# Optimization experiments

Measured on AMD Instinct MI355X. Metric: run time of the kernel, lower is better.

The kernel has to match this reference:

```python
import jax, jax.numpy as jnp
import numpy as np

INTERVAL = 4
UPSCALE = 4
K = 3              # sample_size
SAMPLERS = 3
Q = 2 ** INTERVAL                 # 16
L = 2 ** (8 - INTERVAL) + 1       # 17
PAD = K - 1
B, H, W = 4, 512, 512

_STRIDES = np.array([L ** 3, L ** 2, L, 1], dtype=np.int32)


def ste_round(x):
    # straight-through round (round_func in the torch code)
    return x + jax.lax.stop_gradient(jnp.round(x) - x)


def fix_weight(w):
    return jnp.clip(ste_round(w * 127.0), -127.0, 127.0)


def sample(img, sw, sb):
    # unfold(K, K-1) + conv-per-patch + fold is exactly a VALID conv.
    # img: (B,1,h+PAD,w+PAD); sw: (4,1,K,K) -> a,b,c,d each (B,1,h,w)
    out = jax.lax.conv_general_dilated(img, sw, (1, 1), 'VALID',
        dimension_numbers=('NCHW', 'OIHW', 'NCHW')) + sb[None, :, None, None]
    return out[:, 0:1], out[:, 1:2], out[:, 2:3], out[:, 3:4]


def interp(lut, res_w, sw, sb, scale, img_in, prev_img):
    # InterpTorchBatch: 4D simplex interpolation into the quantized LUT.
    # Sorted-simplex form is equivalent to the 24-case masked torch code
    # (ties yield zero-weight terms, so tie ordering is irrelevant).
    w = fix_weight(lut)                                       # (L^4, scale*scale)
    a, b, c, d = sample(img_in, sw, sb)
    if prev_img is not None:
        rw = jnp.clip(res_w, 0.0, 1.0)
        pa, pb, pc, pd = sample(prev_img, sw, sb)
        a = rw[0, 0] * pa + (1.0 - rw[0, 0]) * a
        b = rw[0, 1] * pb + (1.0 - rw[0, 1]) * b
        c = rw[1, 0] * pc + (1.0 - rw[1, 0]) * c
        d = rw[1, 1] * pd + (1.0 - rw[1, 1]) * d
    vals = jnp.concatenate([a, b, c, d], axis=1).transpose(0, 2, 3, 1)   # (B,h,w,4)
    lo = jnp.floor_divide(vals, float(Q)).astype(jnp.int32)
    f = jnp.mod(vals, float(Q))
    order = jnp.argsort(-f, axis=-1)                          # fractional parts, descending
    fs = jnp.take_along_axis(f, order, axis=-1)
    strides = jnp.asarray(_STRIDES)
    base = jnp.sum(lo * strides, axis=-1)                     # flat index of p0000
    inc = jnp.cumsum(strides[order], axis=-1)
    verts = jnp.concatenate([base[..., None], base[..., None] + inc], axis=-1)  # (B,h,w,5)
    ws = jnp.concatenate([float(Q) - fs[..., :1], fs[..., :-1] - fs[..., 1:], fs[..., -1:]], axis=-1)
    p = w[verts]                                              # gather: (B,h,w,5,scale*scale)
    out = jnp.einsum('bhwv,bhwvk->bhwk', ws, p) / float(Q)
    bb, hh, ww, _ = out.shape
    out = out.reshape(bb, hh, ww, scale, scale).transpose(0, 1, 3, 2, 4)
    return out.reshape(bb, 1, hh * scale, ww * scale)


def _pad_rot(x, r):
    return jnp.pad(jnp.rot90(x, r, axes=(2, 3)),
                   ((0, 0), (0, 0), (0, PAD), (0, PAD)), mode='edge')


def rotate_input(lut, scale, sw, sb, x, res_w, prev_x):
    pred = jnp.zeros((), jnp.float32)
    for r in range(4):
        pr = None if prev_x is None else _pad_rot(prev_x, r)
        pred = pred + jnp.rot90(
            interp(lut, res_w, sw, sb, scale, _pad_rot(x, r), pr),
            (4 - r) % 4, axes=(2, 3))
        pred = ste_round(pred)
    return pred


def autolut_forward(x, lut0, lut1, samp0, samp1, sbias0, sbias1, resw1):
    x = x * 255.0
    # stage 0: scale 1, no residual, bias 127
    pred = 0.0
    for s in range(SAMPLERS):
        pred = pred + rotate_input(lut0[s], 1, samp0[s], sbias0[s], x, None, None)
    prev_x = x
    x = ste_round(jnp.clip(pred / (SAMPLERS * 4.0) + 127.0, 0.0, 255.0))
    # stage 1 (last): upscale, residual blend with previous stage input
    pred = 0.0
    for s in range(SAMPLERS):
        pred = pred + rotate_input(lut1[s], UPSCALE, samp1[s], sbias1[s], x, resw1[s], prev_x)
    x = ste_round(jnp.clip(pred / float(SAMPLERS), 0.0, 255.0))
    return x / 255.0   # phase == 'train'


def setup_inputs() -> dict:
    key = jax.random.key(0)
    ks = jax.random.split(key, 6)
    x = jax.random.uniform(ks[0], (B, 1, H, W), dtype=jnp.float32)
    lut0 = jax.random.uniform(ks[1], (SAMPLERS, L ** 4, 1), jnp.float32, -1.0, 1.0)
    lut1 = jax.random.uniform(ks[2], (SAMPLERS, L ** 4, UPSCALE * UPSCALE), jnp.float32, -1.0, 1.0)

    def mk_sampler(k):
        w = jax.random.normal(k, (SAMPLERS, 4, 1, K, K), dtype=jnp.float32)
        # convex combination of patch pixels -> sampled values stay in [0,255]
        return jax.nn.softmax(w.reshape(SAMPLERS, 4, -1), axis=-1).reshape(SAMPLERS, 4, 1, K, K)

    samp0 = mk_sampler(ks[3])
    samp1 = mk_sampler(ks[4])
    sbias0 = jnp.zeros((SAMPLERS, 4), jnp.float32)
    sbias1 = jnp.zeros((SAMPLERS, 4), jnp.float32)
    resw1 = jax.random.uniform(ks[5], (SAMPLERS, 2, 2), dtype=jnp.float32)
    return {"x": x, "lut0": lut0, "lut1": lut1, "samp0": samp0, "samp1": samp1,
            "sbias0": sbias0, "sbias1": sbias1, "resw1": resw1}


def reference(x, lut0, lut1, samp0, samp1, sbias0, sbias1, resw1):
    return autolut_forward(x, lut0, lut1, samp0, samp1, sbias0, sbias1, resw1)
```

## Files before the change

### kernel.cpp

```cpp
#include <hip/hip_runtime.h>
#include <math.h>

static constexpr int B_ = 4;
static constexpr int N_ = 512;
static constexpr int N4_ = 2048;
static constexpr int NPIX = B_ * N_ * N_;
static constexpr int LUT_ROWS = 83521;
static constexpr int SPAD = 83584;
static constexpr int ST0 = 4913, ST1 = 289, ST2 = 17, ST3 = 1;

__device__ __forceinline__ float fixw(float v) {
    v = rintf(v * 127.0f);
    return fminf(fmaxf(v, -127.0f), 127.0f);
}

__global__ void fix_lut0_kernel(const float* __restrict__ in, char* __restrict__ out) {
    int t = blockIdx.x * blockDim.x + threadIdx.x;
    int s = blockIdx.y;
    if (t < LUT_ROWS) out[(size_t)s * SPAD + t] = (char)(int)fixw(in[(size_t)s * LUT_ROWS + t]);
}

__global__ void fix_lut1_kernel(const float4* __restrict__ in, uchar4* __restrict__ out, int n4) {
    int t = blockIdx.x * blockDim.x + threadIdx.x;
    if (t < n4) {
        float4 v = in[t];
        uchar4 o;
        o.x = (unsigned char)((int)fixw(v.x) + 127);
        o.y = (unsigned char)((int)fixw(v.y) + 127);
        o.z = (unsigned char)((int)fixw(v.z) + 127);
        o.w = (unsigned char)((int)fixw(v.w) + 127);
        out[t] = o;
    }
}

struct Simplex {
    int v[5];
    float w[5];
};

__device__ __forceinline__ double pack_key(float f, unsigned stride) {
    unsigned long long u = ((unsigned long long)__float_as_uint(f) << 32) | stride;
    return __longlong_as_double((long long)u);
}
__device__ __forceinline__ float key_f(double k) {
    return __uint_as_float((unsigned)((unsigned long long)__double_as_longlong(k) >> 32));
}
__device__ __forceinline__ int key_s(double k) {
    return (int)(unsigned)__double_as_longlong(k);
}

__device__ __forceinline__ Simplex simplex4(float a, float b, float c, float d) {
    float fl0 = floorf(a * 0.0625f), fl1 = floorf(b * 0.0625f),
          fl2 = floorf(c * 0.0625f), fl3 = floorf(d * 0.0625f);
    float f0 = a - 16.0f * fl0, f1 = b - 16.0f * fl1,
          f2 = c - 16.0f * fl2, f3 = d - 16.0f * fl3;
    int l0 = min(max((int)fl0, 0), 15);
    int l1 = min(max((int)fl1, 0), 15);
    int l2 = min(max((int)fl2, 0), 15);
    int l3 = min(max((int)fl3, 0), 15);
    double k0 = pack_key(f0, (unsigned)ST0);
    double k1 = pack_key(f1, (unsigned)ST1);
    double k2 = pack_key(f2, (unsigned)ST2);
    double k3 = pack_key(f3, (unsigned)ST3);
#define CSWD(X, Y) { double mx_ = fmax(X, Y); Y = fmin(X, Y); X = mx_; }
    CSWD(k0, k1) CSWD(k2, k3) CSWD(k0, k2) CSWD(k1, k3) CSWD(k1, k2)
#undef CSWD
    Simplex s;
    s.v[0] = l0 * ST0 + l1 * ST1 + l2 * ST2 + l3;
    s.v[1] = s.v[0] + key_s(k0);
    s.v[2] = s.v[1] + key_s(k1);
    s.v[3] = s.v[2] + key_s(k2);
    s.v[4] = s.v[3] + key_s(k3);
    float g0 = key_f(k0), g1 = key_f(k1), g2 = key_f(k2), g3 = key_f(k3);
    s.w[0] = (16.0f - g0) * 0.0625f;
    s.w[1] = (g0 - g1) * 0.0625f;
    s.w[2] = (g1 - g2) * 0.0625f;
    s.w[3] = (g2 - g3) * 0.0625f;
    s.w[4] = g3 * 0.0625f;
    return s;
}

__device__ __forceinline__ bool tap_for_r(int r, int a, int c, int& di, int& dj) {
    if (r == 0) { di = a - 2; dj = c - 2; return (a >= 2) && (c >= 2); }
    if (r == 1) { di = 2 - c; dj = a - 2; return (a >= 2) && (c <= 2); }
    if (r == 2) { di = 2 - a; dj = 2 - c; return (a <= 2) && (c <= 2); }
    di = c - 2; dj = 2 - a; return (a <= 2) && (c >= 2);
}

__device__ __forceinline__ void acc4u(unsigned int q, float wv, float* oc) {
    oc[0] = fmaf(wv, (float)(q & 0xffu), oc[0]);
    oc[1] = fmaf(wv, (float)((q >> 8) & 0xffu), oc[1]);
    oc[2] = fmaf(wv, (float)((q >> 16) & 0xffu), oc[2]);
    oc[3] = fmaf(wv, (float)(q >> 24), oc[3]);
}

__global__ __launch_bounds__(512, 1) void stage0_kernel(
    const float* __restrict__ x,
    const char* __restrict__ lut0q,
    const float* __restrict__ samp0,
    const float* __restrict__ sbias0,
    float* __restrict__ x1)
{
    __shared__ char luts[SPAD];

    int b    = blockIdx.x >> 9;
    int tile = blockIdx.x & 511;
    int i = ((tile >> 4) << 4) + (threadIdx.x >> 5);
    int j = ((tile & 15) << 5) + (threadIdx.x & 31);
    const float* xb = x + (size_t)b * N_ * N_;

    float vals[3][4][4];
    #pragma unroll
    for (int s = 0; s < 3; ++s)
        #pragma unroll
        for (int r = 0; r < 4; ++r)
            #pragma unroll
            for (int ch = 0; ch < 4; ++ch) vals[s][r][ch] = 0.0f;
    #pragma unroll
    for (int a = 0; a < 5; ++a) {
        int ri = min(max(i - 2 + a, 0), N_ - 1);
        const float* row = xb + ri * N_;
        #pragma unroll
        for (int c = 0; c < 5; ++c) {
            int ci = min(max(j - 2 + c, 0), N_ - 1);
            float px = row[ci] * 255.0f;
            #pragma unroll
            for (int r = 0; r < 4; ++r) {
                int di, dj;
                if (tap_for_r(r, a, c, di, dj)) {
                    #pragma unroll
                    for (int s = 0; s < 3; ++s)
                        #pragma unroll
                        for (int ch = 0; ch < 4; ++ch)
                            vals[s][r][ch] += samp0[s * 36 + ch * 9 + di * 3 + dj] * px;
                }
            }
        }
    }

    float pred = 0.0f;
    #pragma unroll
    for (int s = 0; s < 3; ++s) {
        __syncthreads();
        {
            const int4* src = (const int4*)(lut0q + (size_t)s * SPAD);
            int4* dst = (int4*)luts;
            for (int u = threadIdx.x; u < SPAD / 16; u += 512) dst[u] = src[u];
        }
        __syncthreads();

        const float* sb = sbias0 + s * 4;

        Simplex sx[4];
        #pragma unroll
        for (int r = 0; r < 4; ++r)
            sx[r] = simplex4(vals[s][r][0] + sb[0], vals[s][r][1] + sb[1],
                             vals[s][r][2] + sb[2], vals[s][r][3] + sb[3]);

        float p[4][5];
        #pragma unroll
        for (int r = 0; r < 4; ++r)
            #pragma unroll
            for (int v = 0; v < 5; ++v)
                p[r][v] = (float)luts[sx[r].v[v]];

        float acc = 0.0f;
        #pragma unroll
        for (int r = 0; r < 4; ++r) {
            asm volatile("" : "+v"(p[r][0]), "+v"(p[r][1]), "+v"(p[r][2]),
                              "+v"(p[r][3]), "+v"(p[r][4]));
            float o = sx[r].w[0] * p[r][0] + sx[r].w[1] * p[r][1]
                    + sx[r].w[2] * p[r][2] + sx[r].w[3] * p[r][3]
                    + sx[r].w[4] * p[r][4];
            acc = rintf(acc + o);
        }
        pred += acc;
    }
    x1[(size_t)b * N_ * N_ + i * N_ + j] =
        rintf(fminf(fmaxf(pred / 12.0f + 127.0f, 0.0f), 255.0f));
}

__global__ __launch_bounds__(256, 1) void stage1_kernel(
    const float* __restrict__ x,
    const float* __restrict__ x1,
    const unsigned char* __restrict__ lut1q,
    const float* __restrict__ samp1,
    const float* __restrict__ sbias1,
    const float* __restrict__ resw1,
    float* __restrict__ out)
{
    int b    = blockIdx.x >> 10;
    int tile = blockIdx.x & 1023;
    int i = ((tile >> 5) << 4) + (threadIdx.x >> 4);
    int j = ((tile & 31) << 4) + (threadIdx.x & 15);
    const float* xb  = x  + (size_t)b * N_ * N_;
    const float* x1b = x1 + (size_t)b * N_ * N_;

    float tot[16];
    #pragma unroll
    for (int k = 0; k < 16; ++k) tot[k] = 0.0f;

    for (int s = 0; s < 3; ++s) {
        const float* w  = samp1 + s * 36;
        const unsigned char* lut = lut1q + (size_t)s * LUT_ROWS * 16;
        float rws[4];
        #pragma unroll
        for (int ch = 0; ch < 4; ++ch)
            rws[ch] = fminf(fmaxf(resw1[s * 4 + ch], 0.0f), 1.0f);

        float vals[4][4];
        #pragma unroll
        for (int r = 0; r < 4; ++r)
            #pragma unroll
            for (int ch = 0; ch < 4; ++ch) vals[r][ch] = sbias1[s * 4 + ch];

        #pragma unroll
        for (int a = 0; a < 5; ++a) {
            int ri = min(max(i - 2 + a, 0), N_ - 1);
            const float* r1 = x1b + ri * N_;
            const float* r0 = xb + ri * N_;
            #pragma unroll
            for (int c = 0; c < 5; ++c) {
                int ci = min(max(j - 2 + c, 0), N_ - 1);
                float pc = r1[ci];
                float dq = r0[ci] * 255.0f - pc;
                float q[4];
                #pragma unroll
                for (int ch = 0; ch < 4; ++ch)
                    q[ch] = fmaf(rws[ch], dq, pc);
                #pragma unroll
                for (int r = 0; r < 4; ++r) {
                    int di, dj;
                    if (tap_for_r(r, a, c, di, dj)) {
                        #pragma unroll
                        for (int ch = 0; ch < 4; ++ch)
                            vals[r][ch] += w[ch * 9 + di * 3 + dj] * q[ch];
                    }
                }
            }
        }

        Simplex sx[4];
        #pragma unroll
        for (int r = 0; r < 4; ++r)
            sx[r] = simplex4(vals[r][0], vals[r][1], vals[r][2], vals[r][3]);

        uint4 g[4][5];
        #pragma unroll
        for (int r = 0; r < 4; ++r)
            #pragma unroll
            for (int v = 0; v < 5; ++v)
                g[r][v] = *(const uint4*)(lut + (size_t)sx[r].v[v] * 16);

        float acc[16];
        #pragma unroll
        for (int k = 0; k < 16; ++k) acc[k] = 0.0f;

        #pragma unroll
        for (int r = 0; r < 4; ++r) {
            #pragma unroll
            for (int v = 0; v < 5; ++v)
                asm volatile("" : "+v"(g[r][v].x), "+v"(g[r][v].y),
                                  "+v"(g[r][v].z), "+v"(g[r][v].w));
            float oc[16];
            #pragma unroll
            for (int k = 0; k < 16; ++k) oc[k] = 0.0f;
            #pragma unroll
            for (int v = 0; v < 5; ++v) {
                float wv = sx[r].w[v];
                acc4u(g[r][v].x, wv, oc);
                acc4u(g[r][v].y, wv, oc + 4);
                acc4u(g[r][v].z, wv, oc + 8);
                acc4u(g[r][v].w, wv, oc + 12);
            }
            float S = sx[r].w[0] + sx[r].w[1] + sx[r].w[2] + sx[r].w[3] + sx[r].w[4];
            float bias = 127.0f * S;
            #pragma unroll
            for (int k = 0; k < 16; ++k) oc[k] -= bias;
            #pragma unroll
            for (int u = 0; u < 4; ++u)
                #pragma unroll
                for (int v2 = 0; v2 < 4; ++v2) {
                    int k = 4 * u + v2;
                    int c = (r == 0) ? (4 * u + v2)
                          : (r == 1) ? (4 * (3 - v2) + u)
                          : (r == 2) ? (4 * (3 - u) + (3 - v2))
                                     : (4 * v2 + (3 - u));
                    acc[k] = rintf(acc[k] + oc[c]);
                }
        }
        #pragma unroll
        for (int k = 0; k < 16; ++k) tot[k] += acc[k];
    }

    float* ob = out + (size_t)b * N4_ * N4_ + (size_t)(i * 4) * N4_ + (j * 4);
    #pragma unroll
    for (int u = 0; u < 4; ++u) {
        float4 val;
        val.x = rintf(fminf(fmaxf(tot[4 * u + 0] / 3.0f, 0.0f), 255.0f)) * (1.0f / 255.0f);
        val.y = rintf(fminf(fmaxf(tot[4 * u + 1] / 3.0f, 0.0f), 255.0f)) * (1.0f / 255.0f);
        val.z = rintf(fminf(fmaxf(tot[4 * u + 2] / 3.0f, 0.0f), 255.0f)) * (1.0f / 255.0f);
        val.w = rintf(fminf(fmaxf(tot[4 * u + 3] / 3.0f, 0.0f), 255.0f)) * (1.0f / 255.0f);
        *(float4*)(ob + (size_t)u * N4_) = val;
    }
}

extern "C" void kernel_launch(void* const* d_in, const int* in_sizes, int n_in,
                              void* d_out, int out_size, void* d_ws, size_t ws_size,
                              hipStream_t stream) {
    const float* x      = (const float*)d_in[0];
    const float* lut0   = (const float*)d_in[1];
    const float* lut1   = (const float*)d_in[2];
    const float* samp0  = (const float*)d_in[3];
    const float* samp1  = (const float*)d_in[4];
    const float* sbias0 = (const float*)d_in[5];
    const float* sbias1 = (const float*)d_in[6];
    const float* resw1  = (const float*)d_in[7];
    float* out = (float*)d_out;
    char* ws   = (char*)d_ws;

    const int N_L1 = 3 * LUT_ROWS * 16;
    size_t off_x1 = 0;
    size_t off_l0 = (size_t)NPIX * sizeof(float);
    size_t off_l1 = (off_l0 + (size_t)3 * SPAD + 15) & ~(size_t)15;

    float* x1 = (float*)(ws + off_x1);
    char* l0q = ws + off_l0;
    unsigned char* l1q = (unsigned char*)(ws + off_l1);

    const int threads = 256;

    dim3 g0((LUT_ROWS + threads - 1) / threads, 3);
    fix_lut0_kernel<<<g0, threads, 0, stream>>>(lut0, l0q);
    fix_lut1_kernel<<<(N_L1 / 4 + threads - 1) / threads, threads, 0, stream>>>(
        (const float4*)lut1, (uchar4*)l1q, N_L1 / 4);
    stage0_kernel<<<NPIX / 512, 512, 0, stream>>>(x, l0q, samp0, sbias0, x1);
    stage1_kernel<<<NPIX / threads, threads, 0, stream>>>(x, x1, l1q, samp1, sbias1, resw1, out);
}
```

Before: 312.2 us.

## Shrink stage0 LDS table, use direct global-to-LDS loads, fall back to global for tail

Stage0 now keeps only the first 81408 bytes of each quantized LUT in shared memory and copies them with global_load_lds, which writes straight from global memory into LDS without passing through registers. Lookups whose indices fall past that range read the remaining entries from global memory. The launch bound now allows more resident blocks per CU. The smaller LDS footprint is meant to let more blocks share a CU and overlap the table copies, at the cost of a divergent slow path for high indices.

```diff
diff --git a/kernel.cpp b/kernel.cpp
--- a/kernel.cpp
+++ b/kernel.cpp
@@ -8,6 +8,7 @@
 static constexpr int LUT_ROWS = 83521;
 static constexpr int SPAD = 83584;
 static constexpr int ST0 = 4913, ST1 = 289, ST2 = 17, ST3 = 1;
+static constexpr int LDS0 = 81408;
 
 __device__ __forceinline__ float fixw(float v) {
     v = rintf(v * 127.0f);
@@ -94,19 +95,20 @@
     oc[3] = fmaf(wv, (float)(q >> 24), oc[3]);
 }
 
-__global__ __launch_bounds__(512, 1) void stage0_kernel(
+__global__ __launch_bounds__(512, 4) void stage0_kernel(
     const float* __restrict__ x,
     const char* __restrict__ lut0q,
     const float* __restrict__ samp0,
     const float* __restrict__ sbias0,
     float* __restrict__ x1)
 {
-    __shared__ char luts[SPAD];
+    __shared__ char luts[LDS0];
 
     int b    = blockIdx.x >> 9;
     int tile = blockIdx.x & 511;
     int i = ((tile >> 4) << 4) + (threadIdx.x >> 5);
     int j = ((tile & 15) << 5) + (threadIdx.x & 31);
+    const int tid = threadIdx.x;
     const float* xb = x + (size_t)b * N_ * N_;
 
     float vals[3][4][4];
@@ -141,28 +143,47 @@
     float pred = 0.0f;
     #pragma unroll
     for (int s = 0; s < 3; ++s) {
+        const char* lutg = lut0q + (size_t)s * SPAD;
+
         __syncthreads();
-        {
-            const int4* src = (const int4*)(lut0q + (size_t)s * SPAD);
-            int4* dst = (int4*)luts;
-            for (int u = threadIdx.x; u < SPAD / 16; u += 512) dst[u] = src[u];
+        for (int u = tid; u < LDS0 / 16; u += 512) {
+            int off = u * 16;
+            __builtin_amdgcn_global_load_lds(
+                (const __attribute__((address_space(1))) void*)(lutg + off),
+                (__attribute__((address_space(3))) void*)(luts + off),
+                16, 0, 0);
         }
         __syncthreads();
 
         const float* sb = sbias0 + s * 4;
-
         Simplex sx[4];
         #pragma unroll
         for (int r = 0; r < 4; ++r)
             sx[r] = simplex4(vals[s][r][0] + sb[0], vals[s][r][1] + sb[1],
                              vals[s][r][2] + sb[2], vals[s][r][3] + sb[3]);
 
+        int mx = 0;
+        #pragma unroll
+        for (int r = 0; r < 4; ++r)
+            #pragma unroll
+            for (int v = 0; v < 5; ++v) mx = max(mx, sx[r].v[v]);
+
         float p[4][5];
-        #pragma unroll
-        for (int r = 0; r < 4; ++r)
-            #pragma unroll
-            for (int v = 0; v < 5; ++v)
-                p[r][v] = (float)luts[sx[r].v[v]];
+        if (mx < LDS0) {
+            #pragma unroll
+            for (int r = 0; r < 4; ++r)
+                #pragma unroll
+                for (int v = 0; v < 5; ++v)
+                    p[r][v] = (float)luts[sx[r].v[v]];
+        } else {
+            #pragma unroll
+            for (int r = 0; r < 4; ++r)
+                #pragma unroll
+                for (int v = 0; v < 5; ++v) {
+                    int idx = sx[r].v[v];
+                    p[r][v] = (idx < LDS0) ? (float)luts[idx] : (float)lutg[idx];
+                }
+        }
 
         float acc = 0.0f;
         #pragma unroll
```

After: 302.4 us. -3.2%, faster.
